# Kernel tuning notes

Measured on AMD Instinct MI355X. Metric: run time of the kernel, lower is better.

Reference implementation:

```python
import jax, jax.numpy as jnp
import numpy as np

N_NODES = 100000
N_EDGES = 1600000
N_GRAPHS = 256
IN_DIM, HID, OUT_DIM = 20, 128, 30954


def setup_inputs() -> dict:
    key = jax.random.key(0)
    ks = jax.random.split(key, 9)
    x = jax.random.normal(ks[0], (N_NODES, IN_DIM), dtype=jnp.float32)
    edge_index = jax.random.randint(ks[1], (2, N_EDGES), 0, N_NODES, dtype=jnp.int64)
    batch = jnp.sort(jax.random.randint(ks[2], (N_NODES,), 0, N_GRAPHS, dtype=jnp.int64))
    s = 0.05
    W1 = jax.random.normal(ks[3], (IN_DIM, HID), dtype=jnp.float32) * s
    b1 = jax.random.normal(ks[4], (HID,), dtype=jnp.float32) * s
    W2 = jax.random.normal(ks[5], (HID, HID), dtype=jnp.float32) * s
    b2 = jax.random.normal(ks[6], (HID,), dtype=jnp.float32) * s
    Wc = jax.random.normal(ks[7], (HID, OUT_DIM), dtype=jnp.float32) * s
    bc = jax.random.normal(ks[8], (OUT_DIM,), dtype=jnp.float32) * s
    return {"x": x, "edge_index": edge_index, "batch": batch,
            "W1": W1, "b1": b1, "W2": W2, "b2": b2, "Wc": Wc, "bc": bc}


def _gcn_norm(edge_index, n_nodes):
    # add self loops (PyG GCNConv default), symmetric normalization
    loops = jnp.arange(n_nodes, dtype=edge_index.dtype)
    src = jnp.concatenate([edge_index[0], loops])
    dst = jnp.concatenate([edge_index[1], loops])
    deg = jax.ops.segment_sum(jnp.ones_like(dst, dtype=jnp.float32), dst,
                              num_segments=n_nodes)
    dinv = jnp.where(deg > 0, jax.lax.rsqrt(deg), 0.0)
    norm = dinv[src] * dinv[dst]  # [E+N]
    return src, dst, norm


def _gcn_conv(x, src, dst, norm, W, b, n_nodes):
    h = x @ W                              # [N, out] transform first (fewer msg flops)
    msg = h[src] * norm[:, None]           # gather + scale
    out = jax.ops.segment_sum(msg, dst, num_segments=n_nodes)
    return out + b


def reference(x, edge_index, batch, W1, b1, W2, b2, Wc, bc):
    n = x.shape[0]
    src, dst, norm = _gcn_norm(edge_index, n)
    h = jax.nn.relu(_gcn_conv(x, src, dst, norm, W1, b1, n))
    # dropout is identity in eval mode
    h = jax.nn.relu(_gcn_conv(h, src, dst, norm, W2, b2, n))
    # global mean pool per graph
    sums = jax.ops.segment_sum(h, batch, num_segments=N_GRAPHS)       # [G, HID]
    cnts = jax.ops.segment_sum(jnp.ones((n,), jnp.float32), batch,
                               num_segments=N_GRAPHS)
    pooled = sums / jnp.maximum(cnts, 1.0)[:, None]
    return pooled @ Wc + bc  # [G, OUT_DIM]
```

## Files before the change

kernel.cpp:

```cpp
#include <hip/hip_runtime.h>

#define HID 128
#define SCAN_B 256

__device__ __forceinline__ float bf_lo(unsigned int u) { return __uint_as_float(u << 16); }
__device__ __forceinline__ float bf_hi(unsigned int u) { return __uint_as_float(u & 0xFFFF0000u); }
__device__ __forceinline__ unsigned short f2bf(float f) {
    unsigned int u = __float_as_uint(f);
    unsigned int r = (u + 0x7FFFu + ((u >> 16) & 1u)) >> 16;
    return (unsigned short)r;
}

__global__ void init_kernel(const unsigned int* __restrict__ p, int* __restrict__ flag,
                            float4* __restrict__ deg4, long long n4) {
    if (blockIdx.x == 0 && threadIdx.x == 0) {
        int is64 = 1;
        for (int i = 0; i < 64; ++i) {
            if (p[2 * i + 1] != 0u) { is64 = 0; break; }
        }
        *flag = is64;
    }
    long long i = (long long)blockIdx.x * blockDim.x + threadIdx.x;
    long long stride = (long long)gridDim.x * blockDim.x;
    for (; i < n4; i += stride) deg4[i] = make_float4(0.f, 0.f, 0.f, 0.f);
}

__global__ void cvtdeg_kernel(const void* __restrict__ p, int* __restrict__ out,
                              int* __restrict__ deg, int E, const int* __restrict__ flag) {
    int i = blockIdx.x * blockDim.x + threadIdx.x;
    if (i < 2 * E) {
        int v = (*flag) ? (int)((const long long*)p)[i] : ((const int*)p)[i];
        out[i] = v;
        if (i >= E) atomicAdd(&deg[v], 1);
    }
}

__global__ void cvtx_kernel(const float* __restrict__ x, const float* __restrict__ dinv,
                            unsigned short* __restrict__ xb, int n, int IN) {
    int i = blockIdx.x * blockDim.x + threadIdx.x;
    if (i < n) {
        int node = i / IN;
        xb[i] = f2bf(x[i] * dinv[node]);
    }
}

__global__ __launch_bounds__(SCAN_B) void scan1_kernel(const int* __restrict__ deg,
                                                       int* __restrict__ incl,
                                                       int* __restrict__ blockSums, int N) {
    __shared__ int s[SCAN_B];
    int i = blockIdx.x * SCAN_B + threadIdx.x;
    int v = (i < N) ? deg[i] : 0;
    s[threadIdx.x] = v;
    __syncthreads();
#pragma unroll
    for (int off = 1; off < SCAN_B; off <<= 1) {
        int t = (threadIdx.x >= off) ? s[threadIdx.x - off] : 0;
        __syncthreads();
        s[threadIdx.x] += t;
        __syncthreads();
    }
    if (i < N) incl[i] = s[threadIdx.x];
    if (threadIdx.x == SCAN_B - 1) blockSums[blockIdx.x] = s[SCAN_B - 1];
}

__global__ __launch_bounds__(1024) void scan2_kernel(int* __restrict__ blockSums, int nb) {
    __shared__ int s[1024];
    int v = (threadIdx.x < nb) ? blockSums[threadIdx.x] : 0;
    s[threadIdx.x] = v;
    __syncthreads();
#pragma unroll
    for (int off = 1; off < 1024; off <<= 1) {
        int t = (threadIdx.x >= off) ? s[threadIdx.x - off] : 0;
        __syncthreads();
        s[threadIdx.x] += t;
        __syncthreads();
    }
    if (threadIdx.x < nb) blockSums[threadIdx.x] = (threadIdx.x > 0) ? s[threadIdx.x - 1] : 0;
}

__global__ void scan3_kernel(const int* __restrict__ incl, const int* __restrict__ deg,
                             const int* __restrict__ blockSums, int* __restrict__ rowstart,
                             float* __restrict__ dinv, int* __restrict__ cursor,
                             const void* __restrict__ bt, const int* __restrict__ flag,
                             int* __restrict__ gstart, int G,
                             int N, int E) {
    int i = blockIdx.x * blockDim.x + threadIdx.x;
    if (i < N) {
        int d = deg[i];
        rowstart[i] = incl[i] - d + blockSums[i / SCAN_B];
        dinv[i] = rsqrtf((float)(d + 1));
        cursor[i] = 0;
    }
    if (i == 0) rowstart[N] = E;
    if (i <= G) {
        int is64 = *flag;
        int lo = 0, hi = N;
        while (lo < hi) {
            int mid = (lo + hi) >> 1;
            int v = is64 ? (int)((const long long*)bt)[mid] : ((const int*)bt)[mid];
            if (v < i) lo = mid + 1; else hi = mid;
        }
        gstart[i] = lo;
    }
}

__global__ void scatter_kernel(const int* __restrict__ src, const int* __restrict__ dst,
                               const int* __restrict__ rowstart, int* __restrict__ cursor,
                               int2* __restrict__ elist, const float* __restrict__ dinv, int E) {
    int e = blockIdx.x * blockDim.x + threadIdx.x;
    if (e >= E) return;
    int s = src[e], d = dst[e];
    int pos = rowstart[d] + atomicAdd(&cursor[d], 1);
    float nm = dinv[s] * dinv[d];
    elist[pos] = make_int2(s, __float_as_int(nm));
}

__global__ __launch_bounds__(256) void agg_lin1_kernel(const unsigned int* __restrict__ xb32,
                                                       const float* __restrict__ W,
                                                       const float* __restrict__ b,
                                                       unsigned int* __restrict__ h1b,
                                                       const int* __restrict__ rowstart,
                                                       const int2* __restrict__ elist,
                                                       const float* __restrict__ dinv,
                                                       int N, int IN) {
    __shared__ float Ws[20 * HID];
    __shared__ float zs[8][20];
    const int tid = threadIdx.x;
    for (int i = tid; i < IN * HID; i += 256) Ws[i] = W[i];

    const int g      = tid >> 5;
    const int lane32 = tid & 31;
    const int slot   = lane32 >> 4;
    const int l      = lane32 & 15;
    const int node   = blockIdx.x * 8 + g;
    const int half   = IN >> 1;
    const bool act   = (node < N) && (l < half);

    float accx = 0.f, accy = 0.f;
    if (node < N) {
        int beg = rowstart[node], end = rowstart[node + 1];
        int e = beg + slot;
        for (; e + 6 < end; e += 8) {
            int s0 = elist[e].x;
            int s1 = elist[e + 2].x;
            int s2 = elist[e + 4].x;
            int s3 = elist[e + 6].x;
            unsigned int u0 = act ? xb32[(size_t)s0 * half + l] : 0u;
            unsigned int u1 = act ? xb32[(size_t)s1 * half + l] : 0u;
            unsigned int u2 = act ? xb32[(size_t)s2 * half + l] : 0u;
            unsigned int u3 = act ? xb32[(size_t)s3 * half + l] : 0u;
            accx += bf_lo(u0) + bf_lo(u1) + bf_lo(u2) + bf_lo(u3);
            accy += bf_hi(u0) + bf_hi(u1) + bf_hi(u2) + bf_hi(u3);
        }
        for (; e < end; e += 2) {
            int s0 = elist[e].x;
            unsigned int u0 = act ? xb32[(size_t)s0 * half + l] : 0u;
            accx += bf_lo(u0);
            accy += bf_hi(u0);
        }
    }
    accx += __shfl_xor(accx, 16, 64);
    accy += __shfl_xor(accy, 16, 64);
    if (node < N && slot == 0 && l < half) {
        float di = dinv[node];
        unsigned int us = xb32[(size_t)node * half + l];
        zs[g][2 * l]     = di * (accx + bf_lo(us));
        zs[g][2 * l + 1] = di * (accy + bf_hi(us));
    }
    __syncthreads();

    if (node < N) {
        const int j = lane32;
        float4 acc4 = ((const float4*)b)[j];
        for (int k = 0; k < IN; ++k) {
            float zv = zs[g][k];
            float4 w = *(const float4*)&Ws[k * HID + j * 4];
            acc4.x += zv * w.x; acc4.y += zv * w.y;
            acc4.z += zv * w.z; acc4.w += zv * w.w;
        }
        acc4.x = fmaxf(acc4.x, 0.f); acc4.y = fmaxf(acc4.y, 0.f);
        acc4.z = fmaxf(acc4.z, 0.f); acc4.w = fmaxf(acc4.w, 0.f);
        uint2 st;
        st.x = (unsigned)f2bf(acc4.x) | ((unsigned)f2bf(acc4.y) << 16);
        st.y = (unsigned)f2bf(acc4.z) | ((unsigned)f2bf(acc4.w) << 16);
        ((uint2*)h1b)[(size_t)node * 32 + j] = st;
    }
}

#define TBM 64
#define TBN 64
#define TBK 32
#define XLD (TBM + 4)

__global__ __launch_bounds__(256) void gemm128_kernel(const unsigned int* __restrict__ Ab,
                                                      const float* __restrict__ W,
                                                      const float* __restrict__ dinv,
                                                      unsigned short* __restrict__ Cb, int N) {
    __shared__ float xs[TBK][XLD];
    __shared__ float wsh[TBK][TBN + 4];
    const int tid = threadIdx.x;
    const int n0 = blockIdx.x * TBM;
    const int c0 = blockIdx.y * TBN;
    const int ng = tid >> 4;
    const int cg = tid & 15;
    const int anode = tid >> 2;
    const int af    = tid & 3;
    const int wk    = tid >> 4;
    const int wc    = tid & 15;

    const uint4* Av = (const uint4*)Ab;

    float acc[4][4] = {};

    for (int k0 = 0; k0 < HID; k0 += TBK) {
        {
            int gn = n0 + anode;
            uint4 u = make_uint4(0u, 0u, 0u, 0u);
            if (gn < N) u = Av[(size_t)gn * 16 + (k0 >> 3) + af];
            int kb = af * 8;
            xs[kb + 0][anode] = bf_lo(u.x);
            xs[kb + 1][anode] = bf_hi(u.x);
            xs[kb + 2][anode] = bf_lo(u.y);
            xs[kb + 3][anode] = bf_hi(u.y);
            xs[kb + 4][anode] = bf_lo(u.z);
            xs[kb + 5][anode] = bf_hi(u.z);
            xs[kb + 6][anode] = bf_lo(u.w);
            xs[kb + 7][anode] = bf_hi(u.w);
        }
#pragma unroll
        for (int r = 0; r < 2; ++r) {
            int kk = wk + r * 16;
            *(float4*)&wsh[kk][wc * 4] =
                *(const float4*)(W + (size_t)(k0 + kk) * HID + c0 + wc * 4);
        }
        __syncthreads();
#pragma unroll
        for (int kk = 0; kk < TBK; ++kk) {
            float a[4], b[4];
            *(float4*)a = *(const float4*)&xs[kk][ng * 4];
            *(float4*)b = *(const float4*)&wsh[kk][cg * 4];
#pragma unroll
            for (int m = 0; m < 4; ++m)
#pragma unroll
                for (int n = 0; n < 4; ++n) acc[m][n] += a[m] * b[n];
        }
        __syncthreads();
    }

#pragma unroll
    for (int m = 0; m < 4; ++m) {
        int gn = n0 + ng * 4 + m;
        if (gn < N) {
            float di = dinv[gn];
            ushort4 st;
            st.x = f2bf(acc[m][0] * di); st.y = f2bf(acc[m][1] * di);
            st.z = f2bf(acc[m][2] * di); st.w = f2bf(acc[m][3] * di);
            *(ushort4*)(Cb + (size_t)gn * HID + c0 + cg * 4) = st;
        }
    }
}

__global__ __launch_bounds__(256) void csr_aggb_kernel(const unsigned short* __restrict__ h2b,
                                                       unsigned short* __restrict__ outb,
                                                       const int* __restrict__ rowstart,
                                                       const int2* __restrict__ elist,
                                                       const float* __restrict__ dinv,
                                                       const float* __restrict__ bias,
                                                       int N) {
    int node = blockIdx.x * 16 + (threadIdx.x >> 4);
    if (node >= N) return;
    int q = threadIdx.x & 15;
    const uint4* hv = (const uint4*)h2b;
    float acc[8] = {};
    int beg = rowstart[node], end = rowstart[node + 1];
    int e = beg;
    for (; e + 3 < end; e += 4) {
        int s0 = elist[e].x;
        int s1 = elist[e + 1].x;
        int s2 = elist[e + 2].x;
        int s3 = elist[e + 3].x;
        uint4 a0 = hv[(size_t)s0 * 16 + q];
        uint4 a1 = hv[(size_t)s1 * 16 + q];
        uint4 a2 = hv[(size_t)s2 * 16 + q];
        uint4 a3 = hv[(size_t)s3 * 16 + q];
        acc[0] += bf_lo(a0.x) + bf_lo(a1.x) + bf_lo(a2.x) + bf_lo(a3.x);
        acc[1] += bf_hi(a0.x) + bf_hi(a1.x) + bf_hi(a2.x) + bf_hi(a3.x);
        acc[2] += bf_lo(a0.y) + bf_lo(a1.y) + bf_lo(a2.y) + bf_lo(a3.y);
        acc[3] += bf_hi(a0.y) + bf_hi(a1.y) + bf_hi(a2.y) + bf_hi(a3.y);
        acc[4] += bf_lo(a0.z) + bf_lo(a1.z) + bf_lo(a2.z) + bf_lo(a3.z);
        acc[5] += bf_hi(a0.z) + bf_hi(a1.z) + bf_hi(a2.z) + bf_hi(a3.z);
        acc[6] += bf_lo(a0.w) + bf_lo(a1.w) + bf_lo(a2.w) + bf_lo(a3.w);
        acc[7] += bf_hi(a0.w) + bf_hi(a1.w) + bf_hi(a2.w) + bf_hi(a3.w);
    }
    for (; e < end; ++e) {
        int s0 = elist[e].x;
        uint4 a0 = hv[(size_t)s0 * 16 + q];
        acc[0] += bf_lo(a0.x); acc[1] += bf_hi(a0.x);
        acc[2] += bf_lo(a0.y); acc[3] += bf_hi(a0.y);
        acc[4] += bf_lo(a0.z); acc[5] += bf_hi(a0.z);
        acc[6] += bf_lo(a0.w); acc[7] += bf_hi(a0.w);
    }
    float di = dinv[node];
    uint4 sv = hv[(size_t)node * 16 + q];
    float self[8] = { bf_lo(sv.x), bf_hi(sv.x), bf_lo(sv.y), bf_hi(sv.y),
                      bf_lo(sv.z), bf_hi(sv.z), bf_lo(sv.w), bf_hi(sv.w) };
    float4 b0 = ((const float4*)bias)[2 * q];
    float4 b1 = ((const float4*)bias)[2 * q + 1];
    float r[8];
    r[0] = fmaxf(di * (acc[0] + self[0]) + b0.x, 0.f);
    r[1] = fmaxf(di * (acc[1] + self[1]) + b0.y, 0.f);
    r[2] = fmaxf(di * (acc[2] + self[2]) + b0.z, 0.f);
    r[3] = fmaxf(di * (acc[3] + self[3]) + b0.w, 0.f);
    r[4] = fmaxf(di * (acc[4] + self[4]) + b1.x, 0.f);
    r[5] = fmaxf(di * (acc[5] + self[5]) + b1.y, 0.f);
    r[6] = fmaxf(di * (acc[6] + self[6]) + b1.z, 0.f);
    r[7] = fmaxf(di * (acc[7] + self[7]) + b1.w, 0.f);
    uint4 st;
    st.x = (unsigned)f2bf(r[0]) | ((unsigned)f2bf(r[1]) << 16);
    st.y = (unsigned)f2bf(r[2]) | ((unsigned)f2bf(r[3]) << 16);
    st.z = (unsigned)f2bf(r[4]) | ((unsigned)f2bf(r[5]) << 16);
    st.w = (unsigned)f2bf(r[6]) | ((unsigned)f2bf(r[7]) << 16);
    ((uint4*)outb)[(size_t)node * 16 + q] = st;
}

__global__ __launch_bounds__(1024) void pool2_kernel(const unsigned short* __restrict__ hb,
                                                     const int* __restrict__ gstart,
                                                     float* __restrict__ meanp, int G) {
    int g = blockIdx.x;
    int part = threadIdx.x >> 7;
    int j = threadIdx.x & 127;
    int beg = gstart[g], end = gstart[g + 1];
    float s = 0.f;
    for (int n = beg + part; n < end; n += 8)
        s += __uint_as_float(((unsigned)hb[(size_t)n * HID + j]) << 16);
    __shared__ float red[8][HID];
    red[part][j] = s;
    __syncthreads();
    if (part == 0) {
        float tot = 0.f;
#pragma unroll
        for (int r = 0; r < 8; ++r) tot += red[r][j];
        float c = (float)(end - beg);
        meanp[(size_t)g * HID + j] = tot / fmaxf(c, 1.f);
    }
}

#define CBM 64
#define CBN 64
#define CBK 32

__global__ __launch_bounds__(256) void clsgemm_kernel(const float* __restrict__ A,
                                                      const float* __restrict__ Bw,
                                                      const float* __restrict__ bc,
                                                      float* __restrict__ C,
                                                      int G, int OUT) {
    __shared__ float as[CBK][CBM + 4];
    __shared__ float bs[CBK][CBN + 4];
    const int tid = threadIdx.x;
    const int g0 = blockIdx.y * CBM;
    const int c0 = blockIdx.x * CBN;
    const int mg = tid >> 4;
    const int cg = tid & 15;
    const int arow = tid >> 3;
    const int af   = tid & 7;
    const int wk   = tid >> 4;
    const int wc   = tid & 15;

    float acc[4][4] = {};

    for (int k0 = 0; k0 < HID; k0 += CBK) {
#pragma unroll
        for (int r = 0; r < 2; ++r) {
            int row = arow + r * 32;
            int g = g0 + row;
            float4 v = make_float4(0.f, 0.f, 0.f, 0.f);
            if (g < G) v = *(const float4*)(A + (size_t)g * HID + k0 + af * 4);
            as[af * 4 + 0][row] = v.x;
            as[af * 4 + 1][row] = v.y;
            as[af * 4 + 2][row] = v.z;
            as[af * 4 + 3][row] = v.w;
        }
#pragma unroll
        for (int r = 0; r < 2; ++r) {
            int kk = wk + r * 16;
            int c = c0 + wc * 4;
            const float* bp = Bw + (size_t)(k0 + kk) * OUT + c;
            float2 lo = make_float2(0.f, 0.f), hi = make_float2(0.f, 0.f);
            if (c + 3 < OUT) {
                lo = *(const float2*)bp;
                hi = *(const float2*)(bp + 2);
            } else {
                if (c + 0 < OUT) lo.x = bp[0];
                if (c + 1 < OUT) lo.y = bp[1];
                if (c + 2 < OUT) hi.x = bp[2];
                if (c + 3 < OUT) hi.y = bp[3];
            }
            bs[kk][wc * 4 + 0] = lo.x;
            bs[kk][wc * 4 + 1] = lo.y;
            bs[kk][wc * 4 + 2] = hi.x;
            bs[kk][wc * 4 + 3] = hi.y;
        }
        __syncthreads();
#pragma unroll
        for (int kk = 0; kk < CBK; ++kk) {
            float a[4], b[4];
            *(float4*)a = *(const float4*)&as[kk][mg * 4];
            *(float4*)b = *(const float4*)&bs[kk][cg * 4];
#pragma unroll
            for (int m = 0; m < 4; ++m)
#pragma unroll
                for (int n = 0; n < 4; ++n) acc[m][n] += a[m] * b[n];
        }
        __syncthreads();
    }

    int c = c0 + cg * 4;
    float b0 = (c + 0 < OUT) ? bc[c + 0] : 0.f;
    float b1 = (c + 1 < OUT) ? bc[c + 1] : 0.f;
    float b2 = (c + 2 < OUT) ? bc[c + 2] : 0.f;
    float b3 = (c + 3 < OUT) ? bc[c + 3] : 0.f;
#pragma unroll
    for (int m = 0; m < 4; ++m) {
        int g = g0 + mg * 4 + m;
        if (g >= G) continue;
        float* cp = C + (size_t)g * OUT + c;
        if (c + 3 < OUT) {
            *(float2*)cp = make_float2(acc[m][0] + b0, acc[m][1] + b1);
            *(float2*)(cp + 2) = make_float2(acc[m][2] + b2, acc[m][3] + b3);
        } else {
            if (c + 0 < OUT) cp[0] = acc[m][0] + b0;
            if (c + 1 < OUT) cp[1] = acc[m][1] + b1;
            if (c + 2 < OUT) cp[2] = acc[m][2] + b2;
            if (c + 3 < OUT) cp[3] = acc[m][3] + b3;
        }
    }
}

extern "C" void kernel_launch(void* const* d_in, const int* in_sizes, int n_in,
                              void* d_out, int out_size, void* d_ws, size_t ws_size,
                              hipStream_t stream) {
    const float* x  = (const float*)d_in[0];
    const void*  ei = d_in[1];
    const void*  bt = d_in[2];
    const float* W1 = (const float*)d_in[3];
    const float* b1 = (const float*)d_in[4];
    const float* W2 = (const float*)d_in[5];
    const float* b2 = (const float*)d_in[6];
    const float* Wc = (const float*)d_in[7];
    const float* bc = (const float*)d_in[8];
    float* out = (float*)d_out;

    const int N   = in_sizes[2];
    const int E   = in_sizes[1] / 2;
    const int IN  = in_sizes[0] / N;
    const int OUT = in_sizes[8];
    const int G   = out_size / OUT;

    char* ws = (char*)d_ws;
    size_t off = 0;
    auto alloc = [&](size_t bytes) {
        size_t p = off;
        off += (bytes + 255) & ~(size_t)255;
        return p;
    };
    int*            idx32    = (int*)(ws + alloc((size_t)2 * E * 4));
    int*            deg      = (int*)(ws + alloc((size_t)N * 4));
    float*          dinv     = (float*)(ws + alloc((size_t)N * 4));
    int*            incl     = (int*)(ws + alloc((size_t)N * 4));
    int*            rowstart = (int*)(ws + alloc((size_t)(N + 1) * 4));
    int*            cursor   = (int*)(ws + alloc((size_t)N * 4));
    int*            blockSums= (int*)(ws + alloc((size_t)1024 * 4));
    int2*           elist    = (int2*)(ws + alloc((size_t)E * 8));
    unsigned short* xb       = (unsigned short*)(ws + alloc((size_t)N * IN * 2));
    unsigned int*   h1b      = (unsigned int*)(ws + alloc((size_t)N * HID * 2));
    unsigned short* h2b      = (unsigned short*)(ws + alloc((size_t)N * HID * 2));
    unsigned short* houtb    = (unsigned short*)(ws + alloc((size_t)N * HID * 2));
    int*            gstart   = (int*)(ws + alloc((size_t)(G + 1) * 4));
    float*          meanp    = (float*)(ws + alloc((size_t)G * HID * 4));
    int*            flag     = (int*)(ws + alloc(4));
    (void)ws_size;

    int* srcI = idx32;
    int* dstI = idx32 + E;

    const int B = 256;
    const int nb = (N + SCAN_B - 1) / SCAN_B;

    init_kernel<<<256, B, 0, stream>>>((const unsigned int*)ei, flag, (float4*)deg,
                                       (long long)N / 4);
    cvtdeg_kernel<<<(2 * E + B - 1) / B, B, 0, stream>>>(ei, idx32, deg, E, flag);

    scan1_kernel<<<nb, SCAN_B, 0, stream>>>(deg, incl, blockSums, N);
    scan2_kernel<<<1, 1024, 0, stream>>>(blockSums, nb);
    scan3_kernel<<<(N + B - 1) / B, B, 0, stream>>>(incl, deg, blockSums, rowstart,
                                                    dinv, cursor, bt, flag, gstart, G, N, E);
    cvtx_kernel<<<(N * IN + B - 1) / B, B, 0, stream>>>(x, dinv, xb, N * IN, IN);
    scatter_kernel<<<(E + B - 1) / B, B, 0, stream>>>(srcI, dstI, rowstart, cursor, elist, dinv, E);

    agg_lin1_kernel<<<(N + 7) / 8, 256, 0, stream>>>((const unsigned int*)xb, W1, b1,
                                                     h1b, rowstart, elist, dinv, N, IN);

    {
        dim3 grid((N + TBM - 1) / TBM, HID / TBN);
        gemm128_kernel<<<grid, 256, 0, stream>>>(h1b, W2, dinv, h2b, N);
    }
    csr_aggb_kernel<<<(N + 15) / 16, 256, 0, stream>>>(h2b, houtb, rowstart, elist, dinv, b2, N);

    pool2_kernel<<<G, 1024, 0, stream>>>(houtb, gstart, meanp, G);

    {
        dim3 grid((OUT + CBN - 1) / CBN, (G + CBM - 1) / CBM);
        clsgemm_kernel<<<grid, 256, 0, stream>>>(meanp, Wc, bc, out, G, OUT);
    }
}
```

Measured before the change: 371.5 us.

## Fuse x conversion into scan3, deepen gather unrolls, enlarge classifier tile

Folds the bf16 conversion of x (scaled by dinv) into scan3, so each thread converts its own node's row and one launch is removed. Unrolls the edge-gather loops in agg_lin1 and csr_aggb from 4 to 8 loads, giving more memory requests in flight. Doubles the classifier GEMM's M tile to 128 with 8x4 accumulators per thread. Per-thread strided row reads in scan3 coalesce poorly, the larger GEMM tile halves the grid's row dimension and raises register pressure, and the wider unroll leaves more edges to the remainder loop.

```diff
diff --git a/kernel.cpp b/kernel.cpp
--- a/kernel.cpp
+++ b/kernel.cpp
@@ -32,15 +32,6 @@
         int v = (*flag) ? (int)((const long long*)p)[i] : ((const int*)p)[i];
         out[i] = v;
         if (i >= E) atomicAdd(&deg[v], 1);
-    }
-}
-
-__global__ void cvtx_kernel(const float* __restrict__ x, const float* __restrict__ dinv,
-                            unsigned short* __restrict__ xb, int n, int IN) {
-    int i = blockIdx.x * blockDim.x + threadIdx.x;
-    if (i < n) {
-        int node = i / IN;
-        xb[i] = f2bf(x[i] * dinv[node]);
     }
 }
 
@@ -83,13 +74,21 @@
                              float* __restrict__ dinv, int* __restrict__ cursor,
                              const void* __restrict__ bt, const int* __restrict__ flag,
                              int* __restrict__ gstart, int G,
-                             int N, int E) {
+                             const float* __restrict__ x, unsigned int* __restrict__ xb32,
+                             int N, int E, int IN) {
     int i = blockIdx.x * blockDim.x + threadIdx.x;
     if (i < N) {
         int d = deg[i];
         rowstart[i] = incl[i] - d + blockSums[i / SCAN_B];
-        dinv[i] = rsqrtf((float)(d + 1));
+        float di = rsqrtf((float)(d + 1));
+        dinv[i] = di;
         cursor[i] = 0;
+        const float* xr = x + (size_t)i * IN;
+        unsigned int* xo = xb32 + (size_t)i * (IN >> 1);
+        for (int k = 0; k < (IN >> 1); ++k) {
+            float2 v = *(const float2*)(xr + 2 * k);
+            xo[k] = (unsigned)f2bf(v.x * di) | ((unsigned)f2bf(v.y * di) << 16);
+        }
     }
     if (i == 0) rowstart[N] = E;
     if (i <= G) {
@@ -140,17 +139,27 @@
     if (node < N) {
         int beg = rowstart[node], end = rowstart[node + 1];
         int e = beg + slot;
-        for (; e + 6 < end; e += 8) {
+        for (; e + 14 < end; e += 16) {
             int s0 = elist[e].x;
             int s1 = elist[e + 2].x;
             int s2 = elist[e + 4].x;
             int s3 = elist[e + 6].x;
+            int s4 = elist[e + 8].x;
+            int s5 = elist[e + 10].x;
+            int s6 = elist[e + 12].x;
+            int s7 = elist[e + 14].x;
             unsigned int u0 = act ? xb32[(size_t)s0 * half + l] : 0u;
             unsigned int u1 = act ? xb32[(size_t)s1 * half + l] : 0u;
             unsigned int u2 = act ? xb32[(size_t)s2 * half + l] : 0u;
             unsigned int u3 = act ? xb32[(size_t)s3 * half + l] : 0u;
-            accx += bf_lo(u0) + bf_lo(u1) + bf_lo(u2) + bf_lo(u3);
-            accy += bf_hi(u0) + bf_hi(u1) + bf_hi(u2) + bf_hi(u3);
+            unsigned int u4 = act ? xb32[(size_t)s4 * half + l] : 0u;
+            unsigned int u5 = act ? xb32[(size_t)s5 * half + l] : 0u;
+            unsigned int u6 = act ? xb32[(size_t)s6 * half + l] : 0u;
+            unsigned int u7 = act ? xb32[(size_t)s7 * half + l] : 0u;
+            accx += bf_lo(u0) + bf_lo(u1) + bf_lo(u2) + bf_lo(u3)
+                  + bf_lo(u4) + bf_lo(u5) + bf_lo(u6) + bf_lo(u7);
+            accy += bf_hi(u0) + bf_hi(u1) + bf_hi(u2) + bf_hi(u3)
+                  + bf_hi(u4) + bf_hi(u5) + bf_hi(u6) + bf_hi(u7);
         }
         for (; e < end; e += 2) {
             int s0 = elist[e].x;
@@ -274,27 +283,34 @@
     float acc[8] = {};
     int beg = rowstart[node], end = rowstart[node + 1];
     int e = beg;
-    for (; e + 3 < end; e += 4) {
-        int s0 = elist[e].x;
-        int s1 = elist[e + 1].x;
-        int s2 = elist[e + 2].x;
-        int s3 = elist[e + 3].x;
-        uint4 a0 = hv[(size_t)s0 * 16 + q];
-        uint4 a1 = hv[(size_t)s1 * 16 + q];
-        uint4 a2 = hv[(size_t)s2 * 16 + q];
-        uint4 a3 = hv[(size_t)s3 * 16 + q];
-        acc[0] += bf_lo(a0.x) + bf_lo(a1.x) + bf_lo(a2.x) + bf_lo(a3.x);
-        acc[1] += bf_hi(a0.x) + bf_hi(a1.x) + bf_hi(a2.x) + bf_hi(a3.x);
-        acc[2] += bf_lo(a0.y) + bf_lo(a1.y) + bf_lo(a2.y) + bf_lo(a3.y);
-        acc[3] += bf_hi(a0.y) + bf_hi(a1.y) + bf_hi(a2.y) + bf_hi(a3.y);
-        acc[4] += bf_lo(a0.z) + bf_lo(a1.z) + bf_lo(a2.z) + bf_lo(a3.z);
-        acc[5] += bf_hi(a0.z) + bf_hi(a1.z) + bf_hi(a2.z) + bf_hi(a3.z);
-        acc[6] += bf_lo(a0.w) + bf_lo(a1.w) + bf_lo(a2.w) + bf_lo(a3.w);
-        acc[7] += bf_hi(a0.w) + bf_hi(a1.w) + bf_hi(a2.w) + bf_hi(a3.w);
+    for (; e + 7 < end; e += 8) {
+        uint4 a0 = hv[(size_t)elist[e].x * 16 + q];
+        uint4 a1 = hv[(size_t)elist[e + 1].x * 16 + q];
+        uint4 a2 = hv[(size_t)elist[e + 2].x * 16 + q];
+        uint4 a3 = hv[(size_t)elist[e + 3].x * 16 + q];
+        uint4 a4 = hv[(size_t)elist[e + 4].x * 16 + q];
+        uint4 a5 = hv[(size_t)elist[e + 5].x * 16 + q];
+        uint4 a6 = hv[(size_t)elist[e + 6].x * 16 + q];
+        uint4 a7 = hv[(size_t)elist[e + 7].x * 16 + q];
+        acc[0] += bf_lo(a0.x) + bf_lo(a1.x) + bf_lo(a2.x) + bf_lo(a3.x)
+                + bf_lo(a4.x) + bf_lo(a5.x) + bf_lo(a6.x) + bf_lo(a7.x);
+        acc[1] += bf_hi(a0.x) + bf_hi(a1.x) + bf_hi(a2.x) + bf_hi(a3.x)
+                + bf_hi(a4.x) + bf_hi(a5.x) + bf_hi(a6.x) + bf_hi(a7.x);
+        acc[2] += bf_lo(a0.y) + bf_lo(a1.y) + bf_lo(a2.y) + bf_lo(a3.y)
+                + bf_lo(a4.y) + bf_lo(a5.y) + bf_lo(a6.y) + bf_lo(a7.y);
+        acc[3] += bf_hi(a0.y) + bf_hi(a1.y) + bf_hi(a2.y) + bf_hi(a3.y)
+                + bf_hi(a4.y) + bf_hi(a5.y) + bf_hi(a6.y) + bf_hi(a7.y);
+        acc[4] += bf_lo(a0.z) + bf_lo(a1.z) + bf_lo(a2.z) + bf_lo(a3.z)
+                + bf_lo(a4.z) + bf_lo(a5.z) + bf_lo(a6.z) + bf_lo(a7.z);
+        acc[5] += bf_hi(a0.z) + bf_hi(a1.z) + bf_hi(a2.z) + bf_hi(a3.z)
+                + bf_hi(a4.z) + bf_hi(a5.z) + bf_hi(a6.z) + bf_hi(a7.z);
+        acc[6] += bf_lo(a0.w) + bf_lo(a1.w) + bf_lo(a2.w) + bf_lo(a3.w)
+                + bf_lo(a4.w) + bf_lo(a5.w) + bf_lo(a6.w) + bf_lo(a7.w);
+        acc[7] += bf_hi(a0.w) + bf_hi(a1.w) + bf_hi(a2.w) + bf_hi(a3.w)
+                + bf_hi(a4.w) + bf_hi(a5.w) + bf_hi(a6.w) + bf_hi(a7.w);
     }
     for (; e < end; ++e) {
-        int s0 = elist[e].x;
-        uint4 a0 = hv[(size_t)s0 * 16 + q];
+        uint4 a0 = hv[(size_t)elist[e].x * 16 + q];
         acc[0] += bf_lo(a0.x); acc[1] += bf_hi(a0.x);
         acc[2] += bf_lo(a0.y); acc[3] += bf_hi(a0.y);
         acc[4] += bf_lo(a0.z); acc[5] += bf_hi(a0.z);
@@ -345,7 +361,7 @@
     }
 }
 
-#define CBM 64
+#define CBM 128
 #define CBN 64
 #define CBK 32
 
@@ -366,11 +382,11 @@
     const int wk   = tid >> 4;
     const int wc   = tid & 15;
 
-    float acc[4][4] = {};
+    float acc[8][4] = {};
 
     for (int k0 = 0; k0 < HID; k0 += CBK) {
 #pragma unroll
-        for (int r = 0; r < 2; ++r) {
+        for (int r = 0; r < 4; ++r) {
             int row = arow + r * 32;
             int g = g0 + row;
             float4 v = make_float4(0.f, 0.f, 0.f, 0.f);
@@ -403,11 +419,12 @@
         __syncthreads();
 #pragma unroll
         for (int kk = 0; kk < CBK; ++kk) {
-            float a[4], b[4];
-            *(float4*)a = *(const float4*)&as[kk][mg * 4];
+            float a[8], b[4];
+            *(float4*)&a[0] = *(const float4*)&as[kk][mg * 8];
+            *(float4*)&a[4] = *(const float4*)&as[kk][mg * 8 + 4];
             *(float4*)b = *(const float4*)&bs[kk][cg * 4];
 #pragma unroll
-            for (int m = 0; m < 4; ++m)
+            for (int m = 0; m < 8; ++m)
 #pragma unroll
                 for (int n = 0; n < 4; ++n) acc[m][n] += a[m] * b[n];
         }
@@ -420,8 +437,8 @@
     float b2 = (c + 2 < OUT) ? bc[c + 2] : 0.f;
     float b3 = (c + 3 < OUT) ? bc[c + 3] : 0.f;
 #pragma unroll
-    for (int m = 0; m < 4; ++m) {
-        int g = g0 + mg * 4 + m;
+    for (int m = 0; m < 8; ++m) {
+        int g = g0 + mg * 8 + m;
         if (g >= G) continue;
         float* cp = C + (size_t)g * OUT + c;
         if (c + 3 < OUT) {
@@ -493,8 +510,8 @@
     scan1_kernel<<<nb, SCAN_B, 0, stream>>>(deg, incl, blockSums, N);
     scan2_kernel<<<1, 1024, 0, stream>>>(blockSums, nb);
     scan3_kernel<<<(N + B - 1) / B, B, 0, stream>>>(incl, deg, blockSums, rowstart,
-                                                    dinv, cursor, bt, flag, gstart, G, N, E);
-    cvtx_kernel<<<(N * IN + B - 1) / B, B, 0, stream>>>(x, dinv, xb, N * IN, IN);
+                                                    dinv, cursor, bt, flag, gstart, G,
+                                                    x, (unsigned int*)xb, N, E, IN);
     scatter_kernel<<<(E + B - 1) / B, B, 0, stream>>>(srcI, dstI, rowstart, cursor, elist, dinv, E);
 
     agg_lin1_kernel<<<(N + 7) / 8, 256, 0, stream>>>((const unsigned int*)xb, W1, b1,
```

After: 384.7 us. 1.04x slower.
